# Optimization experiments

Measured on AMD Instinct MI355X. Metric: run time of the kernel, lower is better.

## Reference

```python
import jax, jax.numpy as jnp
import numpy as np

N = 50000      # nodes
E = 800000     # edges (before self-loops)
IN = 128       # in_channels
HID = 32       # hidden_channels per head
H = 4          # in_head
OUT = 40       # out_channels
OH = 1         # out_head
NEG = 0.2      # GATConv default negative_slope
EPS = 1e-5     # BatchNorm eps
SKIP = 0.5     # skip_coefficient


def setup_inputs() -> dict:
    key = jax.random.key(0)
    ks = jax.random.split(key, 24)
    s = 0.1
    f32 = jnp.float32
    return dict(
        x=jax.random.normal(ks[0], (N, IN), dtype=f32),
        W0=jax.random.normal(ks[1], (H * HID, IN), dtype=f32) * s,
        as0=jax.random.normal(ks[2], (H, HID), dtype=f32) * s,
        ad0=jax.random.normal(ks[3], (H, HID), dtype=f32) * s,
        b0=jnp.zeros((H * HID,), f32),
        g0=jnp.ones((H * HID,), f32),
        be0=jnp.zeros((H * HID,), f32),
        W1=jax.random.normal(ks[4], (H * HID, H * HID), dtype=f32) * s,
        as1=jax.random.normal(ks[5], (H, HID), dtype=f32) * s,
        ad1=jax.random.normal(ks[6], (H, HID), dtype=f32) * s,
        b1=jnp.zeros((H * HID,), f32),
        g1=jnp.ones((H * HID,), f32),
        be1=jnp.zeros((H * HID,), f32),
        W2=jax.random.normal(ks[7], (OH * OUT, H * HID), dtype=f32) * s,
        as2=jax.random.normal(ks[8], (OH, OUT), dtype=f32) * s,
        ad2=jax.random.normal(ks[9], (OH, OUT), dtype=f32) * s,
        b2=jnp.zeros((OH * OUT,), f32),
        edge_index=jax.random.randint(ks[10], (2, E), 0, N, dtype=jnp.int64),
    )


def gat_layer(x, src, dst, W, a_s, a_d, b, heads, ch):
    # PyG GATConv (concat=True): per-head linear, edge LeakyReLU attention,
    # softmax over incoming edges per destination node, scatter-add aggregate.
    n = x.shape[0]
    h = (x @ W.T).reshape(n, heads, ch)            # [N,H,C]
    al_s = jnp.einsum('nhc,hc->nh', h, a_s)        # [N,H]
    al_d = jnp.einsum('nhc,hc->nh', h, a_d)
    e = jax.nn.leaky_relu(al_s[src] + al_d[dst], NEG)   # [Etot,H]
    m = jax.ops.segment_max(e, dst, num_segments=n)     # per-dst max (stable softmax)
    ex = jnp.exp(e - m[dst])
    denom = jax.ops.segment_sum(ex, dst, num_segments=n)
    alpha = ex / denom[dst]                              # [Etot,H]
    out = jax.ops.segment_sum(alpha[:, :, None] * h[src], dst, num_segments=n)
    return out.reshape(n, heads * ch) + b


def batchnorm(x, g, b):
    # BatchNorm1d, batch-statistics form
    mu = x.mean(0)
    var = x.var(0)
    return (x - mu) * jax.lax.rsqrt(var + EPS) * g + b


def reference(x, W0, as0, ad0, b0, g0, be0, W1, as1, ad1, b1, g1, be1,
              W2, as2, ad2, b2, edge_index):
    loops = jnp.arange(N, dtype=edge_index.dtype)   # GATConv add_self_loops=True
    src = jnp.concatenate([edge_index[0], loops])
    dst = jnp.concatenate([edge_index[1], loops])
    h = jax.nn.relu(batchnorm(gat_layer(x, src, dst, W0, as0, ad0, b0, H, HID), g0, be0))
    skip = h
    h = gat_layer(h, src, dst, W1, as1, ad1, b1, H, HID)
    h = jax.nn.relu(batchnorm(h, g1, be1) + SKIP * skip)
    return gat_layer(h, src, dst, W2, as2, ad2, b2, OH, OUT)
```

## Files before the change

### kernel.cpp

```cpp
#include <hip/hip_runtime.h>
#include <hip/hip_bf16.h>
#include <stdint.h>

#define N_NODES 50000
#define N_EDGES 800000
#define TOT_EDGES (N_EDGES + N_NODES)
#define DIM 128
#define NEG 0.2f
#define BN_EPS 1e-5f
#define SKIPC 0.5f
#define NB 196
#define BCAP 6144

typedef __attribute__((ext_vector_type(8))) short short8;
typedef __attribute__((ext_vector_type(4))) float f32x4;

__device__ inline float bf2f(__hip_bfloat16 v) { return __bfloat162float(v); }
__device__ inline float u16f(unsigned short u) { return __uint_as_float(((unsigned int)u) << 16); }
__device__ inline unsigned short f2bu(float f) {
    __hip_bfloat16 b = __float2bfloat16(f);
    return *(unsigned short*)&b;
}
__device__ inline void fma8(float* acc, float ex, uint4 u) {
    acc[0] += ex * u16f((unsigned short)(u.x & 0xFFFFu));
    acc[1] += ex * u16f((unsigned short)(u.x >> 16));
    acc[2] += ex * u16f((unsigned short)(u.y & 0xFFFFu));
    acc[3] += ex * u16f((unsigned short)(u.y >> 16));
    acc[4] += ex * u16f((unsigned short)(u.z & 0xFFFFu));
    acc[5] += ex * u16f((unsigned short)(u.z >> 16));
    acc[6] += ex * u16f((unsigned short)(u.w & 0xFFFFu));
    acc[7] += ex * u16f((unsigned short)(u.w >> 16));
}
__device__ inline unsigned int pk2(float a, float b) {
    return (unsigned int)f2bu(a) | ((unsigned int)f2bu(b) << 16);
}

__global__ void zero_out_k(unsigned short* out, int n) {
    int g = blockIdx.x * 256 + threadIdx.x;
    if (g < n) out[g] = 0;
}

__global__ void fdetect_k(const unsigned int* __restrict__ w0, int* __restrict__ fflag) {
    __shared__ int cs;
    if (threadIdx.x == 0) cs = 0;
    __syncthreads();
    unsigned int w = w0[threadIdx.x];
    float v0 = u16f((unsigned short)(w & 0xFFFFu));
    float a = fabsf(v0);
    int sane = (a < 2.0f && (a > 1e-20f || v0 == 0.0f)) ? 1 : 0;
    atomicAdd(&cs, sane);
    __syncthreads();
    if (threadIdx.x == 0) fflag[0] = (cs >= 128) ? 1 : 0;
}

__global__ __launch_bounds__(256) void binA_k(const int* __restrict__ ei,
                                              int* __restrict__ bcnt,
                                              unsigned int* __restrict__ pairs) {
    __shared__ int cnt[NB], base[NB], cur[NB];
    __shared__ int sf;
    int t = threadIdx.x;
    if (t == 0) sf = 0;
    for (int i = t; i < NB; i += 256) cnt[i] = 0;
    __syncthreads();
    if (t < 16 && ei[2 * t + 1] != 0) atomicOr(&sf, 1);
    __syncthreads();
    int f = (sf == 0);
    int b0 = blockIdx.x * 4096;
    unsigned int pk[16];
    int bk[16];
    #pragma unroll
    for (int j = 0; j < 16; ++j) {
        int g = b0 + j * 256 + t;
        bk[j] = -1;
        if (g < N_EDGES) {
            int s, d;
            if (f) { s = ei[2 * g]; d = ei[2 * (N_EDGES + g)]; }
            else   { s = ei[g];     d = ei[N_EDGES + g]; }
            if ((unsigned)d < N_NODES && (unsigned)s < N_NODES) {
                bk[j] = d >> 8;
                pk[j] = (unsigned int)s | ((unsigned int)(d & 255) << 16);
                atomicAdd(&cnt[bk[j]], 1);
            }
        }
    }
    __syncthreads();
    if (t < NB) {
        int c = cnt[t];
        base[t] = c ? atomicAdd(&bcnt[t], c) : 0;
        cur[t] = 0;
    }
    __syncthreads();
    #pragma unroll
    for (int j = 0; j < 16; ++j) {
        if (bk[j] >= 0) {
            int off = base[bk[j]] + atomicAdd(&cur[bk[j]], 1);
            if (off < BCAP) pairs[(size_t)bk[j] * BCAP + off] = pk[j];
        }
    }
}

__global__ __launch_bounds__(256) void bucketscan_k(const int* __restrict__ bcnt,
                                                    int* __restrict__ bbase,
                                                    int* __restrict__ row_ptr) {
    __shared__ int sm[256];
    int t = threadIdx.x;
    int v = 0;
    if (t < NB) {
        int nn = min(256, N_NODES - t * 256);
        v = min(bcnt[t], BCAP) + nn;
    }
    sm[t] = v;
    __syncthreads();
    for (int off = 1; off < 256; off <<= 1) {
        int x = (t >= off) ? sm[t - off] : 0;
        __syncthreads();
        sm[t] += x;
        __syncthreads();
    }
    if (t < NB) bbase[t] = sm[t] - v;
    if (t == 255) row_ptr[N_NODES] = sm[255];
}

__global__ __launch_bounds__(256) void binB_k(const int* __restrict__ bcnt,
                                              const int* __restrict__ bbase,
                                              const unsigned int* __restrict__ pairs,
                                              int* __restrict__ row_ptr,
                                              int* __restrict__ ssrc) {
    __shared__ int cntL[256], scanL[256], curL[256];
    int b = blockIdx.x, t = threadIdx.x;
    int n0 = b * 256;
    int nn = min(256, N_NODES - n0);
    int cnt_b = min(bcnt[b], BCAP);
    const unsigned int* P = pairs + (size_t)b * BCAP;
    cntL[t] = (t < nn) ? 1 : 0;
    __syncthreads();
    for (int i = t; i < cnt_b; i += 256)
        atomicAdd(&cntL[P[i] >> 16], 1);
    __syncthreads();
    int v = cntL[t];
    scanL[t] = v;
    __syncthreads();
    for (int off = 1; off < 256; off <<= 1) {
        int x = (t >= off) ? scanL[t - off] : 0;
        __syncthreads();
        scanL[t] += x;
        __syncthreads();
    }
    int excl = scanL[t] - v;
    int gbase = bbase[b];
    if (t < nn) row_ptr[n0 + t] = gbase + excl;
    curL[t] = excl;
    __syncthreads();
    if (t < nn) {
        int pos = atomicAdd(&curL[t], 1);
        ssrc[gbase + pos] = n0 + t;
    }
    for (int i = t; i < cnt_b; i += 256) {
        unsigned int p = P[i];
        int pos = atomicAdd(&curL[p >> 16], 1);
        ssrc[gbase + pos] = (int)(p & 0xFFFFu);
    }
}

struct PrepJobs { const void* src[13]; float* dst[13]; int n[13]; };
__global__ __launch_bounds__(256) void wcvt_k(const void* __restrict__ W0,
                                              const void* __restrict__ W1,
                                              const void* __restrict__ W2,
                                              unsigned short* __restrict__ Wb0,
                                              unsigned short* __restrict__ Wb1,
                                              unsigned short* __restrict__ Wb2,
                                              PrepJobs jobs,
                                              const int* __restrict__ fflag) {
    int f = fflag[0];
    int b = blockIdx.x;
    if (b < 148) {
        int g = b * 256 + threadIdx.x;
        const void* W; unsigned short* Wb; int idx;
        if (g < 16384)        { W = W0; Wb = Wb0; idx = g; }
        else if (g < 32768)   { W = W1; Wb = Wb1; idx = g - 16384; }
        else if (g < 37888)   { W = W2; Wb = Wb2; idx = g - 32768; }
        else return;
        if (f) Wb[idx] = ((const unsigned short*)W)[idx];
        else   Wb[idx] = f2bu(((const float*)W)[idx]);
    } else {
        int j = b - 148;
        int n = jobs.n[j];
        const void* s = jobs.src[j];
        float* d = jobs.dst[j];
        for (int i = threadIdx.x; i < n; i += 256)
            d[i] = f ? bf2f(((const __hip_bfloat16*)s)[i]) : ((const float*)s)[i];
    }
}

__global__ __launch_bounds__(256) void wext_k(unsigned short* __restrict__ Wb0,
                                              unsigned short* __restrict__ Wb1,
                                              unsigned short* __restrict__ Wb2,
                                              const float* __restrict__ pAs0, const float* __restrict__ pAd0,
                                              const float* __restrict__ pAs1, const float* __restrict__ pAd1,
                                              const float* __restrict__ pAs2, const float* __restrict__ pAd2) {
    int g = blockIdx.x * 256 + threadIdx.x;
    if (g < 2048) {
        int layer = g >> 10;
        int gi = g & 1023;
        int rowq = gi >> 7;
        int k = gi & 127;
        int hh = rowq & 3, dir = rowq >> 2;
        unsigned short* Wb = layer ? Wb1 : Wb0;
        const float* p = layer ? (dir ? pAd1 : pAs1) : (dir ? pAd0 : pAs0);
        float v = 0.f;
        #pragma unroll
        for (int c = 0; c < 32; ++c)
            v += p[hh * 32 + c] * u16f(Wb[(size_t)(hh * 32 + c) * 128 + k]);
        Wb[(size_t)(128 + dir * 4 + hh) * 128 + k] = f2bu(v);
    } else if (g < 2304) {
        int gi = g - 2048;
        int dir = gi >> 7;
        int k = gi & 127;
        const float* p = dir ? pAd2 : pAs2;
        float v = 0.f;
        #pragma unroll
        for (int c = 0; c < 40; ++c)
            v += p[c] * u16f(Wb2[(size_t)c * 128 + k]);
        Wb2[(size_t)(40 + dir) * 128 + k] = f2bu(v);
    }
}

template<int MT, int MV, int ALBASE, int NH, bool BF16IN>
__device__ inline void mfma_body(const unsigned short* __restrict__ Xb,
                                 const float* __restrict__ Xf,
                                 const unsigned short* __restrict__ Wb,
                                 unsigned short* __restrict__ Y,
                                 float* __restrict__ als, float* __restrict__ ald, int n) {
    const int MROWS = ALBASE + 2 * NH;
    int wave = (blockIdx.x * blockDim.x + threadIdx.x) >> 6;
    int r0 = wave * 16;
    if (r0 >= n) return;
    int lane = threadIdx.x & 63;
    int m = lane & 15, quad = lane >> 4;
    f32x4 acc[MT];
    #pragma unroll
    for (int t = 0; t < MT; ++t) acc[t] = (f32x4){0.f, 0.f, 0.f, 0.f};
    int arow = min(r0 + m, n - 1);

    #pragma unroll
    for (int kc = 0; kc < 4; ++kc) {
        int k0 = kc * 32 + quad * 8;
        short8 a;
        if (BF16IN) {
            a = *(const short8*)(Xb + (size_t)arow * 128 + k0);
        } else {
            const float* xp = Xf + (size_t)arow * 128 + k0;
            float4 x0 = *(const float4*)xp;
            float4 x1 = *(const float4*)(xp + 4);
            a[0] = (short)f2bu(x0.x); a[1] = (short)f2bu(x0.y);
            a[2] = (short)f2bu(x0.z); a[3] = (short)f2bu(x0.w);
            a[4] = (short)f2bu(x1.x); a[5] = (short)f2bu(x1.y);
            a[6] = (short)f2bu(x1.z); a[7] = (short)f2bu(x1.w);
        }
        #pragma unroll
        for (int t = 0; t < MT; ++t) {
            int col = t * 16 + m;
            short8 b;
            if (col < MROWS) b = *(const short8*)(Wb + (size_t)col * 128 + k0);
            else             b = (short8){0,0,0,0,0,0,0,0};
            acc[t] = __builtin_amdgcn_mfma_f32_16x16x32_bf16(a, b, acc[t], 0, 0, 0);
        }
    }

    #pragma unroll
    for (int t = 0; t < MT; ++t) {
        int col = t * 16 + m;
        #pragma unroll
        for (int r = 0; r < 4; ++r) {
            int row = r0 + quad * 4 + r;
            if (row >= n) continue;
            if (col < MV) {
                Y[(size_t)row * MV + col] = f2bu(acc[t][r]);
            } else if (col < ALBASE + NH) {
                als[row * NH + (col - ALBASE)] = acc[t][r];
            } else if (col < ALBASE + 2 * NH) {
                ald[row * NH + (col - ALBASE - NH)] = acc[t][r];
            }
        }
    }
}

__global__ __launch_bounds__(256) void mfma_x_k(const void* __restrict__ X,
                                                const unsigned short* __restrict__ Wb,
                                                unsigned short* __restrict__ Y,
                                                float* __restrict__ als, float* __restrict__ ald,
                                                int n, const int* __restrict__ fflag) {
    if (fflag[0]) mfma_body<9, 128, 128, 4, true>((const unsigned short*)X, nullptr, Wb, Y, als, ald, n);
    else          mfma_body<9, 128, 128, 4, false>(nullptr, (const float*)X, Wb, Y, als, ald, n);
}

__global__ __launch_bounds__(256) void mfma_b_k(const unsigned short* __restrict__ X,
                                                const unsigned short* __restrict__ Wb,
                                                unsigned short* __restrict__ Y,
                                                float* __restrict__ als, float* __restrict__ ald, int n) {
    mfma_body<9, 128, 128, 4, true>(X, nullptr, Wb, Y, als, ald, n);
}

__global__ __launch_bounds__(256) void mfma_b40_k(const unsigned short* __restrict__ X,
                                                  const unsigned short* __restrict__ Wb,
                                                  unsigned short* __restrict__ Y,
                                                  float* __restrict__ als, float* __restrict__ ald, int n) {
    mfma_body<3, 40, 40, 1, true>(X, nullptr, Wb, Y, als, ald, n);
}

template<int H, int C, int LPG, int CPL, bool FINAL>
__global__ __launch_bounds__(256) void agg4_k(const unsigned short* __restrict__ hbuf,
                                              const float* __restrict__ als,
                                              const float* __restrict__ ald,
                                              const float* __restrict__ bias,
                                              const int* __restrict__ row_ptr,
                                              const int* __restrict__ ssrc,
                                              void* __restrict__ out,
                                              const int* __restrict__ fflag, int n) {
    const int HC = H * C;
    const int G = 64 / LPG;
    const int NV = CPL / 8;
    int gw = (blockIdx.x * blockDim.x + threadIdx.x) >> 6;
    if (gw >= n) return;
    int lane = threadIdx.x & 63;
    int grp = lane / LPG;
    int sl  = lane % LPG;
    int c0 = sl * CPL;
    bool act = c0 < HC;
    int hl = act ? (c0 / C) : 0;
    int d = gw;
    int beg = row_ptr[d], end = row_ptr[d + 1];
    float adh = ald[d * H + hl];

    float denom = 0.f;
    float acc[CPL];
    #pragma unroll
    for (int j = 0; j < CPL; ++j) acc[j] = 0.f;

    int i0 = beg + grp;
    bool h0 = i0 < end;
    bool h1 = (i0 + G) < end;
    float al0 = 0.f, al1 = 0.f;
    uint4 u0[NV], u1[NV];
    if (h0) {
        int s = ssrc[i0];
        al0 = als[s * H + hl];
        if (act) {
            const uint4* hp = (const uint4*)(hbuf + (size_t)s * HC + c0);
            #pragma unroll
            for (int v = 0; v < NV; ++v) u0[v] = hp[v];
        }
    }
    if (h1) {
        int s = ssrc[i0 + G];
        al1 = als[s * H + hl];
        if (act) {
            const uint4* hp = (const uint4*)(hbuf + (size_t)s * HC + c0);
            #pragma unroll
            for (int v = 0; v < NV; ++v) u1[v] = hp[v];
        }
    }
    int inext = i0 + 2 * G;

    while (h0) {
        bool h2 = inext < end;
        float al2 = 0.f;
        uint4 u2[NV];
        if (h2) {
            int s = ssrc[inext];
            al2 = als[s * H + hl];
            if (act) {
                const uint4* hp = (const uint4*)(hbuf + (size_t)s * HC + c0);
                #pragma unroll
                for (int v = 0; v < NV; ++v) u2[v] = hp[v];
            }
        }
        float t = al0 + adh;
        t = t > 0.f ? t : NEG * t;
        float ex = __expf(t);
        denom += ex;
        if (act) {
            #pragma unroll
            for (int v = 0; v < NV; ++v) fma8(acc + v * 8, ex, u0[v]);
        }
        h0 = h1; al0 = al1;
        #pragma unroll
        for (int v = 0; v < NV; ++v) u0[v] = u1[v];
        h1 = h2; al1 = al2;
        #pragma unroll
        for (int v = 0; v < NV; ++v) u1[v] = u2[v];
        inext += G;
    }

    #pragma unroll
    for (int off = LPG; off < 64; off <<= 1) {
        denom += __shfl_xor(denom, off, 64);
        #pragma unroll
        for (int j = 0; j < CPL; ++j) acc[j] += __shfl_xor(acc[j], off, 64);
    }

    if (grp == 0 && act) {
        float inv = 1.f / denom;
        float vals[CPL];
        #pragma unroll
        for (int j = 0; j < CPL; ++j) vals[j] = acc[j] * inv + bias[c0 + j];
        if (FINAL && !fflag[0]) {
            float* of = (float*)out + (size_t)d * HC + c0;
            #pragma unroll
            for (int j = 0; j < CPL; ++j) of[j] = vals[j];
        } else {
            unsigned short* ob = (unsigned short*)out + (size_t)d * HC + c0;
            #pragma unroll
            for (int v = 0; v < NV; ++v) {
                uint4 pk;
                pk.x = pk2(vals[v * 8 + 0], vals[v * 8 + 1]);
                pk.y = pk2(vals[v * 8 + 2], vals[v * 8 + 3]);
                pk.z = pk2(vals[v * 8 + 4], vals[v * 8 + 5]);
                pk.w = pk2(vals[v * 8 + 6], vals[v * 8 + 7]);
                *(uint4*)(ob + v * 8) = pk;
            }
        }
    }
}

__global__ __launch_bounds__(256) void bn_stats_k(const unsigned short* __restrict__ x,
                                                  float* __restrict__ sum,
                                                  float* __restrict__ sumsq, int n) {
    __shared__ float ss[256], sq[256];
    int t = threadIdx.x;
    int c = t & 127, half = t >> 7;
    float s = 0.f, s2 = 0.f;
    for (int r = blockIdx.x * 2 + half; r < n; r += gridDim.x * 2) {
        float v = u16f(x[(size_t)r * 128 + c]);
        s += v; s2 += v * v;
    }
    ss[t] = s; sq[t] = s2;
    __syncthreads();
    if (t < 128) {
        s = ss[t] + ss[t + 128];
        s2 = sq[t] + sq[t + 128];
        atomicAdd(&sum[c], s);
        atomicAdd(&sumsq[c], s2);
    }
}

__global__ void bn_apply_k(const unsigned short* __restrict__ x,
                           const unsigned short* __restrict__ skip,
                           unsigned short* __restrict__ y,
                           const float* __restrict__ sum, const float* __restrict__ sumsq,
                           const float* __restrict__ g, const float* __restrict__ be, int n) {
    int gid = blockIdx.x * 256 + threadIdx.x;
    if (gid >= n * 32) return;
    int e0 = gid * 4;
    int c0 = e0 & 127;
    const float invN = 1.f / (float)N_NODES;
    float4 gg = *(const float4*)(g + c0);
    float4 bb = *(const float4*)(be + c0);
    float4 sm = *(const float4*)(sum + c0);
    float4 sq = *(const float4*)(sumsq + c0);
    ushort4 xv = *(const ushort4*)(x + e0);
    float vx[4] = { u16f(xv.x), u16f(xv.y), u16f(xv.z), u16f(xv.w) };
    float mg[4] = { gg.x, gg.y, gg.z, gg.w };
    float mb[4] = { bb.x, bb.y, bb.z, bb.w };
    float ms[4] = { sm.x, sm.y, sm.z, sm.w };
    float mq[4] = { sq.x, sq.y, sq.z, sq.w };
    float sk[4] = { 0.f, 0.f, 0.f, 0.f };
    if (skip) {
        ushort4 sv = *(const ushort4*)(skip + e0);
        sk[0] = u16f(sv.x); sk[1] = u16f(sv.y); sk[2] = u16f(sv.z); sk[3] = u16f(sv.w);
    }
    unsigned short o[4];
    #pragma unroll
    for (int j = 0; j < 4; ++j) {
        float mean = ms[j] * invN;
        float var = fmaxf(mq[j] * invN - mean * mean, 0.f);
        float inv = rsqrtf(var + BN_EPS);
        float v = (vx[j] - mean) * inv * mg[j] + mb[j];
        if (skip) v += SKIPC * sk[j];
        o[j] = f2bu(fmaxf(v, 0.f));
    }
    *(ushort4*)(y + e0) = make_ushort4(o[0], o[1], o[2], o[3]);
}

extern "C" void kernel_launch(void* const* d_in, const int* in_sizes, int n_in,
                              void* d_out, int out_size, void* d_ws, size_t ws_size,
                              hipStream_t stream) {
    const void* x   = d_in[0];
    const void* W0  = d_in[1];
    const void* as0 = d_in[2];
    const void* ad0 = d_in[3];
    const void* b0  = d_in[4];
    const void* g0  = d_in[5];
    const void* be0 = d_in[6];
    const void* W1  = d_in[7];
    const void* as1 = d_in[8];
    const void* ad1 = d_in[9];
    const void* b1  = d_in[10];
    const void* g1  = d_in[11];
    const void* be1 = d_in[12];
    const void* W2  = d_in[13];
    const void* as2 = d_in[14];
    const void* ad2 = d_in[15];
    const void* b2  = d_in[16];
    const int* ei = (const int*)d_in[17];

    char* w = (char*)d_ws;
    size_t off = 0;
    auto alloc = [&](size_t bytes) -> void* {
        void* p = w + off;
        off = (off + bytes + 255) & ~(size_t)255;
        return p;
    };
    unsigned short* hAgg = (unsigned short*)alloc((size_t)N_NODES * 128 * 2);
    unsigned short* hbf  = (unsigned short*)alloc((size_t)N_NODES * 128 * 2);
    unsigned short* hS   = (unsigned short*)alloc((size_t)N_NODES * 128 * 2);
    unsigned short* hI   = (unsigned short*)alloc((size_t)N_NODES * 128 * 2);
    float* als = (float*)alloc((size_t)N_NODES * 4 * 4);
    float* ald = (float*)alloc((size_t)N_NODES * 4 * 4);
    unsigned short* Wb0 = (unsigned short*)alloc((size_t)136 * 128 * 2);
    unsigned short* Wb1 = (unsigned short*)alloc((size_t)136 * 128 * 2);
    unsigned short* Wb2 = (unsigned short*)alloc((size_t)42 * 128 * 2);
    float* prm = (float*)alloc(2048 * 4);
    int* zreg = (int*)alloc((size_t)(NB + 512) * 4);
    int* bcnt = zreg;
    float* bn0 = (float*)(zreg + NB);
    float* bn1 = bn0 + 256;
    int* row_ptr = (int*)alloc((size_t)(N_NODES + 1) * 4);
    int* ssrc    = (int*)alloc((size_t)TOT_EDGES * 4);
    unsigned int* pairs = (unsigned int*)alloc((size_t)NB * BCAP * 4);
    int* bbase   = (int*)alloc((size_t)NB * 4);
    int* fflag   = (int*)alloc(256);

    float* pAs0 = prm + 0,   * pAd0 = prm + 128,  * pB0 = prm + 256;
    float* pG0  = prm + 384, * pBe0 = prm + 512;
    float* pAs1 = prm + 640, * pAd1 = prm + 768,  * pB1 = prm + 896;
    float* pG1  = prm + 1024,* pBe1 = prm + 1152;
    float* pAs2 = prm + 1280,* pAd2 = prm + 1320, * pB2 = prm + 1360;

    if (off > ws_size) {
        zero_out_k<<<(out_size + 255) / 256, 256, 0, stream>>>((unsigned short*)d_out, out_size);
        return;
    }

    const int MB = (((N_NODES + 15) / 16) + 3) / 4;
    const int AB = (N_NODES * 64 + 255) / 256;
    const int XB4 = (N_NODES * 32 + 255) / 256;

    fdetect_k<<<1, 256, 0, stream>>>((const unsigned int*)W0, fflag);
    hipMemsetAsync(zreg, 0, (size_t)(NB + 512) * 4, stream);
    binA_k<<<(N_EDGES + 4095) / 4096, 256, 0, stream>>>(ei, bcnt, pairs);
    bucketscan_k<<<1, 256, 0, stream>>>(bcnt, bbase, row_ptr);
    binB_k<<<NB, 256, 0, stream>>>(bcnt, bbase, pairs, row_ptr, ssrc);

    PrepJobs jobs;
    const void* srcs[13] = { as0, ad0, b0, g0, be0, as1, ad1, b1, g1, be1, as2, ad2, b2 };
    float* dsts[13] = { pAs0, pAd0, pB0, pG0, pBe0, pAs1, pAd1, pB1, pG1, pBe1, pAs2, pAd2, pB2 };
    int ns[13] = { 128,128,128,128,128, 128,128,128,128,128, 40,40,40 };
    for (int i = 0; i < 13; ++i) { jobs.src[i] = srcs[i]; jobs.dst[i] = dsts[i]; jobs.n[i] = ns[i]; }
    wcvt_k<<<161, 256, 0, stream>>>(W0, W1, W2, Wb0, Wb1, Wb2, jobs, fflag);
    wext_k<<<9, 256, 0, stream>>>(Wb0, Wb1, Wb2, pAs0, pAd0, pAs1, pAd1, pAs2, pAd2);

    mfma_x_k<<<MB, 256, 0, stream>>>(x, Wb0, hbf, als, ald, N_NODES, fflag);
    agg4_k<4, 32, 8, 16, false><<<AB, 256, 0, stream>>>(hbf, als, ald, pB0, row_ptr, ssrc, hAgg, fflag, N_NODES);
    bn_stats_k<<<256, 256, 0, stream>>>(hAgg, bn0, bn0 + 128, N_NODES);
    bn_apply_k<<<XB4, 256, 0, stream>>>(hAgg, nullptr, hS, bn0, bn0 + 128, pG0, pBe0, N_NODES);

    mfma_b_k<<<MB, 256, 0, stream>>>(hS, Wb1, hbf, als, ald, N_NODES);
    agg4_k<4, 32, 8, 16, false><<<AB, 256, 0, stream>>>(hbf, als, ald, pB1, row_ptr, ssrc, hAgg, fflag, N_NODES);
    bn_stats_k<<<256, 256, 0, stream>>>(hAgg, bn1, bn1 + 128, N_NODES);
    bn_apply_k<<<XB4, 256, 0, stream>>>(hAgg, hS, hI, bn1, bn1 + 128, pG1, pBe1, N_NODES);

    mfma_b40_k<<<MB, 256, 0, stream>>>(hI, Wb2, hbf, als, ald, N_NODES);
    agg4_k<1, 40, 8, 8, true><<<AB, 256, 0, stream>>>(hbf, als, ald, pB2, row_ptr, ssrc, d_out, fflag, N_NODES);
}
```

Baseline: 366.7 us.

## Fuse batchnorm apply into next GEMM prologue and drop tiny scan/detect kernels

Removes the standalone bn_apply kernels and folds the BatchNorm affine, ReLU and skip-combine into the A-operand load of the following MFMA GEMM. The skip term is recomputed from the layer-0 aggregate. It also folds the bucket prefix scan into binB, where each block reduces the counts of earlier buckets, and folds format detection into wcvt_k. Together these save several launches and two full N×128 read/write passes, at the cost of extra per-element ALU work and a redundant small reduction in every block.

```diff
diff --git a/kernel.cpp b/kernel.cpp
--- a/kernel.cpp
+++ b/kernel.cpp
@@ -38,19 +38,6 @@
 __global__ void zero_out_k(unsigned short* out, int n) {
     int g = blockIdx.x * 256 + threadIdx.x;
     if (g < n) out[g] = 0;
-}
-
-__global__ void fdetect_k(const unsigned int* __restrict__ w0, int* __restrict__ fflag) {
-    __shared__ int cs;
-    if (threadIdx.x == 0) cs = 0;
-    __syncthreads();
-    unsigned int w = w0[threadIdx.x];
-    float v0 = u16f((unsigned short)(w & 0xFFFFu));
-    float a = fabsf(v0);
-    int sane = (a < 2.0f && (a > 1e-20f || v0 == 0.0f)) ? 1 : 0;
-    atomicAdd(&cs, sane);
-    __syncthreads();
-    if (threadIdx.x == 0) fflag[0] = (cs >= 128) ? 1 : 0;
 }
 
 __global__ __launch_bounds__(256) void binA_k(const int* __restrict__ ei,
@@ -99,38 +86,28 @@
     }
 }
 
-__global__ __launch_bounds__(256) void bucketscan_k(const int* __restrict__ bcnt,
-                                                    int* __restrict__ bbase,
-                                                    int* __restrict__ row_ptr) {
-    __shared__ int sm[256];
-    int t = threadIdx.x;
-    int v = 0;
-    if (t < NB) {
-        int nn = min(256, N_NODES - t * 256);
-        v = min(bcnt[t], BCAP) + nn;
-    }
-    sm[t] = v;
-    __syncthreads();
-    for (int off = 1; off < 256; off <<= 1) {
-        int x = (t >= off) ? sm[t - off] : 0;
-        __syncthreads();
-        sm[t] += x;
-        __syncthreads();
-    }
-    if (t < NB) bbase[t] = sm[t] - v;
-    if (t == 255) row_ptr[N_NODES] = sm[255];
-}
-
 __global__ __launch_bounds__(256) void binB_k(const int* __restrict__ bcnt,
-                                              const int* __restrict__ bbase,
                                               const unsigned int* __restrict__ pairs,
                                               int* __restrict__ row_ptr,
                                               int* __restrict__ ssrc) {
     __shared__ int cntL[256], scanL[256], curL[256];
+    __shared__ int sred[256];
     int b = blockIdx.x, t = threadIdx.x;
     int n0 = b * 256;
     int nn = min(256, N_NODES - n0);
     int cnt_b = min(bcnt[b], BCAP);
+    int contrib = 0;
+    if (t < b) contrib = min(bcnt[t], BCAP) + min(256, N_NODES - t * 256);
+    sred[t] = contrib;
+    __syncthreads();
+    #pragma unroll
+    for (int off = 128; off > 0; off >>= 1) {
+        if (t < off) sred[t] += sred[t + off];
+        __syncthreads();
+    }
+    int gbase = sred[0];
+    if (b == NB - 1 && t == 0) row_ptr[N_NODES] = gbase + cnt_b + nn;
+
     const unsigned int* P = pairs + (size_t)b * BCAP;
     cntL[t] = (t < nn) ? 1 : 0;
     __syncthreads();
@@ -147,7 +124,6 @@
         __syncthreads();
     }
     int excl = scanL[t] - v;
-    int gbase = bbase[b];
     if (t < nn) row_ptr[n0 + t] = gbase + excl;
     curL[t] = excl;
     __syncthreads();
@@ -170,11 +146,24 @@
                                               unsigned short* __restrict__ Wb1,
                                               unsigned short* __restrict__ Wb2,
                                               PrepJobs jobs,
-                                              const int* __restrict__ fflag) {
-    int f = fflag[0];
+                                              int* __restrict__ fflag) {
+    __shared__ int cs;
+    int t = threadIdx.x;
+    if (t == 0) cs = 0;
+    __syncthreads();
+    {
+        unsigned int w = ((const unsigned int*)W0)[t];
+        float v0 = u16f((unsigned short)(w & 0xFFFFu));
+        float a = fabsf(v0);
+        int sane = (a < 2.0f && (a > 1e-20f || v0 == 0.0f)) ? 1 : 0;
+        atomicAdd(&cs, sane);
+    }
+    __syncthreads();
+    int f = (cs >= 128) ? 1 : 0;
     int b = blockIdx.x;
+    if (b == 0 && t == 0) fflag[0] = f;
     if (b < 148) {
-        int g = b * 256 + threadIdx.x;
+        int g = b * 256 + t;
         const void* W; unsigned short* Wb; int idx;
         if (g < 16384)        { W = W0; Wb = Wb0; idx = g; }
         else if (g < 32768)   { W = W1; Wb = Wb1; idx = g - 16384; }
@@ -187,7 +176,7 @@
         int n = jobs.n[j];
         const void* s = jobs.src[j];
         float* d = jobs.dst[j];
-        for (int i = threadIdx.x; i < n; i += 256)
+        for (int i = t; i < n; i += 256)
             d[i] = f ? bf2f(((const __hip_bfloat16*)s)[i]) : ((const float*)s)[i];
     }
 }
@@ -225,13 +214,37 @@
     }
 }
 
-template<int MT, int MV, int ALBASE, int NH, bool BF16IN>
-__device__ inline void mfma_body(const unsigned short* __restrict__ Xb,
-                                 const float* __restrict__ Xf,
+template<int MT, int MV, int ALBASE, int NH, int AMODE>
+__device__ inline void mfma_body(const void* __restrict__ X,
+                                 const unsigned short* __restrict__ Xprev,
                                  const unsigned short* __restrict__ Wb,
                                  unsigned short* __restrict__ Y,
-                                 float* __restrict__ als, float* __restrict__ ald, int n) {
+                                 float* __restrict__ als, float* __restrict__ ald, int n,
+                                 const float* __restrict__ bnA, const float* __restrict__ gA,
+                                 const float* __restrict__ beA,
+                                 const float* __restrict__ bnB, const float* __restrict__ gB,
+                                 const float* __restrict__ beB) {
     const int MROWS = ALBASE + 2 * NH;
+    __shared__ float sAsc[128], sAsh[128], sBsc[128], sBsh[128];
+    if (AMODE >= 2) {
+        int t = threadIdx.x;
+        const float invN = 1.f / (float)N_NODES;
+        if (t < 128) {
+            float mean = bnA[t] * invN;
+            float var = fmaxf(bnA[128 + t] * invN - mean * mean, 0.f);
+            float s = rsqrtf(var + BN_EPS) * gA[t];
+            sAsc[t] = s;
+            sAsh[t] = beA[t] - mean * s;
+        } else if (AMODE == 3) {
+            int c = t - 128;
+            float mean = bnB[c] * invN;
+            float var = fmaxf(bnB[128 + c] * invN - mean * mean, 0.f);
+            float s = rsqrtf(var + BN_EPS) * gB[c];
+            sBsc[c] = s;
+            sBsh[c] = beB[c] - mean * s;
+        }
+        __syncthreads();
+    }
     int wave = (blockIdx.x * blockDim.x + threadIdx.x) >> 6;
     int r0 = wave * 16;
     if (r0 >= n) return;
@@ -246,16 +259,32 @@
     for (int kc = 0; kc < 4; ++kc) {
         int k0 = kc * 32 + quad * 8;
         short8 a;
-        if (BF16IN) {
-            a = *(const short8*)(Xb + (size_t)arow * 128 + k0);
-        } else {
-            const float* xp = Xf + (size_t)arow * 128 + k0;
+        if (AMODE == 0) {
+            const float* xp = (const float*)X + (size_t)arow * 128 + k0;
             float4 x0 = *(const float4*)xp;
             float4 x1 = *(const float4*)(xp + 4);
             a[0] = (short)f2bu(x0.x); a[1] = (short)f2bu(x0.y);
             a[2] = (short)f2bu(x0.z); a[3] = (short)f2bu(x0.w);
             a[4] = (short)f2bu(x1.x); a[5] = (short)f2bu(x1.y);
             a[6] = (short)f2bu(x1.z); a[7] = (short)f2bu(x1.w);
+        } else if (AMODE == 1) {
+            a = *(const short8*)((const unsigned short*)X + (size_t)arow * 128 + k0);
+        } else if (AMODE == 2) {
+            short8 hv = *(const short8*)((const unsigned short*)X + (size_t)arow * 128 + k0);
+            #pragma unroll
+            for (int j = 0; j < 8; ++j) {
+                float v = u16f((unsigned short)hv[j]) * sAsc[k0 + j] + sAsh[k0 + j];
+                a[j] = (short)f2bu(fmaxf(v, 0.f));
+            }
+        } else {
+            short8 hv = *(const short8*)((const unsigned short*)X + (size_t)arow * 128 + k0);
+            short8 pv = *(const short8*)(Xprev + (size_t)arow * 128 + k0);
+            #pragma unroll
+            for (int j = 0; j < 8; ++j) {
+                float v0 = fmaxf(u16f((unsigned short)pv[j]) * sBsc[k0 + j] + sBsh[k0 + j], 0.f);
+                float v = u16f((unsigned short)hv[j]) * sAsc[k0 + j] + sAsh[k0 + j] + SKIPC * v0;
+                a[j] = (short)f2bu(fmaxf(v, 0.f));
+            }
         }
         #pragma unroll
         for (int t = 0; t < MT; ++t) {
@@ -290,22 +319,38 @@
                                                 unsigned short* __restrict__ Y,
                                                 float* __restrict__ als, float* __restrict__ ald,
                                                 int n, const int* __restrict__ fflag) {
-    if (fflag[0]) mfma_body<9, 128, 128, 4, true>((const unsigned short*)X, nullptr, Wb, Y, als, ald, n);
-    else          mfma_body<9, 128, 128, 4, false>(nullptr, (const float*)X, Wb, Y, als, ald, n);
-}
-
-__global__ __launch_bounds__(256) void mfma_b_k(const unsigned short* __restrict__ X,
-                                                const unsigned short* __restrict__ Wb,
-                                                unsigned short* __restrict__ Y,
-                                                float* __restrict__ als, float* __restrict__ ald, int n) {
-    mfma_body<9, 128, 128, 4, true>(X, nullptr, Wb, Y, als, ald, n);
-}
-
-__global__ __launch_bounds__(256) void mfma_b40_k(const unsigned short* __restrict__ X,
+    if (fflag[0]) mfma_body<9, 128, 128, 4, 1>(X, nullptr, Wb, Y, als, ald, n,
+                                               nullptr, nullptr, nullptr, nullptr, nullptr, nullptr);
+    else          mfma_body<9, 128, 128, 4, 0>(X, nullptr, Wb, Y, als, ald, n,
+                                               nullptr, nullptr, nullptr, nullptr, nullptr, nullptr);
+}
+
+__global__ __launch_bounds__(256) void mfma_aff_k(const unsigned short* __restrict__ X,
                                                   const unsigned short* __restrict__ Wb,
                                                   unsigned short* __restrict__ Y,
-                                                  float* __restrict__ als, float* __restrict__ ald, int n) {
-    mfma_body<3, 40, 40, 1, true>(X, nullptr, Wb, Y, als, ald, n);
+                                                  float* __restrict__ als, float* __restrict__ ald,
+                                                  int n,
+                                                  const float* __restrict__ bn,
+                                                  const float* __restrict__ g,
+                                                  const float* __restrict__ be) {
+    mfma_body<9, 128, 128, 4, 2>(X, nullptr, Wb, Y, als, ald, n,
+                                 bn, g, be, nullptr, nullptr, nullptr);
+}
+
+__global__ __launch_bounds__(256) void mfma_affskip_k(const unsigned short* __restrict__ X,
+                                                      const unsigned short* __restrict__ Xprev,
+                                                      const unsigned short* __restrict__ Wb,
+                                                      unsigned short* __restrict__ Y,
+                                                      float* __restrict__ als, float* __restrict__ ald,
+                                                      int n,
+                                                      const float* __restrict__ bnA,
+                                                      const float* __restrict__ gA,
+                                                      const float* __restrict__ beA,
+                                                      const float* __restrict__ bnB,
+                                                      const float* __restrict__ gB,
+                                                      const float* __restrict__ beB) {
+    mfma_body<3, 40, 40, 1, 3>(X, Xprev, Wb, Y, als, ald, n,
+                               bnA, gA, beA, bnB, gB, beB);
 }
 
 template<int H, int C, int LPG, int CPL, bool FINAL>
@@ -444,44 +489,6 @@
     }
 }
 
-__global__ void bn_apply_k(const unsigned short* __restrict__ x,
-                           const unsigned short* __restrict__ skip,
-                           unsigned short* __restrict__ y,
-                           const float* __restrict__ sum, const float* __restrict__ sumsq,
-                           const float* __restrict__ g, const float* __restrict__ be, int n) {
-    int gid = blockIdx.x * 256 + threadIdx.x;
-    if (gid >= n * 32) return;
-    int e0 = gid * 4;
-    int c0 = e0 & 127;
-    const float invN = 1.f / (float)N_NODES;
-    float4 gg = *(const float4*)(g + c0);
-    float4 bb = *(const float4*)(be + c0);
-    float4 sm = *(const float4*)(sum + c0);
-    float4 sq = *(const float4*)(sumsq + c0);
-    ushort4 xv = *(const ushort4*)(x + e0);
-    float vx[4] = { u16f(xv.x), u16f(xv.y), u16f(xv.z), u16f(xv.w) };
-    float mg[4] = { gg.x, gg.y, gg.z, gg.w };
-    float mb[4] = { bb.x, bb.y, bb.z, bb.w };
-    float ms[4] = { sm.x, sm.y, sm.z, sm.w };
-    float mq[4] = { sq.x, sq.y, sq.z, sq.w };
-    float sk[4] = { 0.f, 0.f, 0.f, 0.f };
-    if (skip) {
-        ushort4 sv = *(const ushort4*)(skip + e0);
-        sk[0] = u16f(sv.x); sk[1] = u16f(sv.y); sk[2] = u16f(sv.z); sk[3] = u16f(sv.w);
-    }
-    unsigned short o[4];
-    #pragma unroll
-    for (int j = 0; j < 4; ++j) {
-        float mean = ms[j] * invN;
-        float var = fmaxf(mq[j] * invN - mean * mean, 0.f);
-        float inv = rsqrtf(var + BN_EPS);
-        float v = (vx[j] - mean) * inv * mg[j] + mb[j];
-        if (skip) v += SKIPC * sk[j];
-        o[j] = f2bu(fmaxf(v, 0.f));
-    }
-    *(ushort4*)(y + e0) = make_ushort4(o[0], o[1], o[2], o[3]);
-}
-
 extern "C" void kernel_launch(void* const* d_in, const int* in_sizes, int n_in,
                               void* d_out, int out_size, void* d_ws, size_t ws_size,
                               hipStream_t stream) {
@@ -511,10 +518,9 @@
         off = (off + bytes + 255) & ~(size_t)255;
         return p;
     };
-    unsigned short* hAgg = (unsigned short*)alloc((size_t)N_NODES * 128 * 2);
-    unsigned short* hbf  = (unsigned short*)alloc((size_t)N_NODES * 128 * 2);
-    unsigned short* hS   = (unsigned short*)alloc((size_t)N_NODES * 128 * 2);
-    unsigned short* hI   = (unsigned short*)alloc((size_t)N_NODES * 128 * 2);
+    unsigned short* hbf = (unsigned short*)alloc((size_t)N_NODES * 128 * 2);
+    unsigned short* hA0 = (unsigned short*)alloc((size_t)N_NODES * 128 * 2);
+    unsigned short* hA1 = (unsigned short*)alloc((size_t)N_NODES * 128 * 2);
     float* als = (float*)alloc((size_t)N_NODES * 4 * 4);
     float* ald = (float*)alloc((size_t)N_NODES * 4 * 4);
     unsigned short* Wb0 = (unsigned short*)alloc((size_t)136 * 128 * 2);
@@ -528,7 +534,6 @@
     int* row_ptr = (int*)alloc((size_t)(N_NODES + 1) * 4);
     int* ssrc    = (int*)alloc((size_t)TOT_EDGES * 4);
     unsigned int* pairs = (unsigned int*)alloc((size_t)NB * BCAP * 4);
-    int* bbase   = (int*)alloc((size_t)NB * 4);
     int* fflag   = (int*)alloc(256);
 
     float* pAs0 = prm + 0,   * pAd0 = prm + 128,  * pB0 = prm + 256;
@@ -544,13 +549,10 @@
 
     const int MB = (((N_NODES + 15) / 16) + 3) / 4;
     const int AB = (N_NODES * 64 + 255) / 256;
-    const int XB4 = (N_NODES * 32 + 255) / 256;
-
-    fdetect_k<<<1, 256, 0, stream>>>((const unsigned int*)W0, fflag);
+
     hipMemsetAsync(zreg, 0, (size_t)(NB + 512) * 4, stream);
     binA_k<<<(N_EDGES + 4095) / 4096, 256, 0, stream>>>(ei, bcnt, pairs);
-    bucketscan_k<<<1, 256, 0, stream>>>(bcnt, bbase, row_ptr);
-    binB_k<<<NB, 256, 0, stream>>>(bcnt, bbase, pairs, row_ptr, ssrc);
+    binB_k<<<NB, 256, 0, stream>>>(bcnt, pairs, row_ptr, ssrc);
 
     PrepJobs jobs;
     const void* srcs[13] = { as0, ad0, b0, g0, be0, as1, ad1, b1, g1, be1, as2, ad2, b2 };
@@ -561,15 +563,14 @@
     wext_k<<<9, 256, 0, stream>>>(Wb0, Wb1, Wb2, pAs0, pAd0, pAs1, pAd1, pAs2, pAd2);
 
     mfma_x_k<<<MB, 256, 0, stream>>>(x, Wb0, hbf, als, ald, N_NODES, fflag);
-    agg4_k<4, 32, 8, 16, false><<<AB, 256, 0, stream>>>(hbf, als, ald, pB0, row_ptr, ssrc, hAgg, fflag, N_NODES);
-    bn_stats_k<<<256, 256, 0, stream>>>(hAgg, bn0, bn0 + 128, N_NODES);
-    bn_apply_k<<<XB4, 256, 0, stream>>>(hAgg, nullptr, hS, bn0, bn0 + 128, pG0, pBe0, N_NODES);
-
-    mfma_b_k<<<MB, 256, 0, stream>>>(hS, Wb1, hbf, als, ald, N_NODES);
-    agg4_k<4, 32, 8, 16, false><<<AB, 256, 0, stream>>>(hbf, als, ald, pB1, row_ptr, ssrc, hAgg, fflag, N_NODES);
-    bn_stats_k<<<256, 256, 0, stream>>>(hAgg, bn1, bn1 + 128, N_NODES);
-    bn_apply_k<<<XB4, 256, 0, stream>>>(hAgg, hS, hI, bn1, bn1 + 128, pG1, pBe1, N_NODES);
-
-    mfma_b40_k<<<MB, 256, 0, stream>>>(hI, Wb2, hbf, als, ald, N_NODES);
+    agg4_k<4, 32, 8, 16, false><<<AB, 256, 0, stream>>>(hbf, als, ald, pB0, row_ptr, ssrc, hA0, fflag, N_NODES);
+    bn_stats_k<<<256, 256, 0, stream>>>(hA0, bn0, bn0 + 128, N_NODES);
+
+    mfma_aff_k<<<MB, 256, 0, stream>>>(hA0, Wb1, hbf, als, ald, N_NODES, bn0, pG0, pBe0);
+    agg4_k<4, 32, 8, 16, false><<<AB, 256, 0, stream>>>(hbf, als, ald, pB1, row_ptr, ssrc, hA1, fflag, N_NODES);
+    bn_stats_k<<<256, 256, 0, stream>>>(hA1, bn1, bn1 + 128, N_NODES);
+
+    mfma_affskip_k<<<MB, 256, 0, stream>>>(hA1, hA0, Wb2, hbf, als, ald, N_NODES,
+                                           bn1, pG1, pBe1, bn0, pG0, pBe0);
     agg4_k<1, 40, 8, 8, true><<<AB, 256, 0, stream>>>(hbf, als, ald, pB2, row_ptr, ssrc, d_out, fflag, N_NODES);
 }
```

Measured after the change: 350.9 us. -4.3%, faster.
